# Optimization experiments

Measured on AMD Instinct MI355X. Metric: run time of the kernel, lower is better.

The kernel has to match this reference:

```python
import jax, jax.numpy as jnp
import numpy as np

N_NODES = 50000
N_EDGES = 800000
IN_C = 128
OUT_C = 128
HEADS = 1
BN_EPS = 1e-5


def setup_inputs() -> dict:
    key = jax.random.key(0)
    k1, k2, k3, k4, k5 = jax.random.split(key, 5)
    x = jax.random.normal(k1, (N_NODES, IN_C), dtype=jnp.float32)
    embedding = jax.random.normal(k2, (N_NODES, OUT_C), dtype=jnp.float32)
    # edges with no self loops (module strips then re-adds self loops)
    dst = jax.random.randint(k3, (N_EDGES,), 0, N_NODES)
    off = jax.random.randint(k4, (N_EDGES,), 1, N_NODES)
    src = (dst + off) % N_NODES
    edge_index = jnp.stack([src, dst]).astype(jnp.int64)
    # parameters
    W = jax.random.normal(k5, (HEADS * OUT_C, IN_C), dtype=jnp.float32) * (1.0 / np.sqrt(IN_C))
    bias = jnp.zeros((HEADS * OUT_C,), dtype=jnp.float32)
    gamma = jnp.ones((HEADS * OUT_C,), dtype=jnp.float32)
    beta = jnp.zeros((HEADS * OUT_C,), dtype=jnp.float32)
    return {"x": x, "edge_index": edge_index, "embedding": embedding,
            "W": W, "bias": bias, "gamma": gamma, "beta": beta}


def reference(x, edge_index, embedding, W, bias, gamma, beta):
    N = x.shape[0]
    xl = x @ W.T  # [N, H*C]
    # add self loops (input edges contain none)
    loop = jnp.arange(N, dtype=edge_index.dtype)
    src = jnp.concatenate([edge_index[0], loop])  # j (source)
    dst = jnp.concatenate([edge_index[1], loop])  # i (target / aggregation index)
    # per-edge attention: cosine-sim style embedding dot product (scalar, shared over heads)
    alpha = jnp.sum(embedding[dst] * embedding[src], axis=-1)  # [Etot]
    # segment softmax over destination neighborhoods
    amax = jax.ops.segment_max(alpha, dst, num_segments=N)
    e = jnp.exp(alpha - amax[dst])
    denom = jax.ops.segment_sum(e, dst, num_segments=N)
    a = e / (denom[dst] + 1e-16)  # [Etot]
    # gather-scale-scatter aggregation
    msg = xl[src] * a[:, None]  # [Etot, H*C]
    out = jax.ops.segment_sum(msg, dst, num_segments=N) + bias  # [N, H*C]
    # BatchNorm1d (training mode: batch stats, biased variance) + ReLU
    mu = out.mean(axis=0)
    var = jnp.mean((out - mu) ** 2, axis=0)
    out = (out - mu) * jax.lax.rsqrt(var + BN_EPS) * gamma + beta
    return jnp.maximum(out, 0.0)
```

## Files before the change

kernel.cpp:

```cpp
#include <hip/hip_runtime.h>
#include <math.h>

#define C 128

typedef _Float16 f16x8 __attribute__((ext_vector_type(8)));
typedef _Float16 half2_t __attribute__((ext_vector_type(2)));
typedef __attribute__((ext_vector_type(4))) float f32x4;

static __device__ __forceinline__ unsigned int pkh2(float lo, float hi) {
    unsigned short l = __builtin_bit_cast(unsigned short, (_Float16)lo);
    unsigned short h = __builtin_bit_cast(unsigned short, (_Float16)hi);
    return ((unsigned int)h << 16) | l;
}
static __device__ __forceinline__ float h2f_lo(unsigned int u) {
    return (float)__builtin_bit_cast(_Float16, (unsigned short)(u & 0xFFFFu));
}
static __device__ __forceinline__ float h2f_hi(unsigned int u) {
    return (float)__builtin_bit_cast(_Float16, (unsigned short)(u >> 16));
}
static __device__ __forceinline__ float dot2acc(unsigned int a, unsigned int b, float c) {
#if __has_builtin(__builtin_amdgcn_fdot2)
    return __builtin_amdgcn_fdot2(__builtin_bit_cast(half2_t, a),
                                  __builtin_bit_cast(half2_t, b), c, false);
#else
    c = fmaf(h2f_lo(a), h2f_lo(b), c);
    return fmaf(h2f_hi(a), h2f_hi(b), c);
#endif
}

__global__ __launch_bounds__(256) void k_stageA(const float* __restrict__ x,
                                                const float* __restrict__ Wf0,
                                                const uint4* __restrict__ wb,
                                                unsigned short* __restrict__ xlh,
                                                const float* __restrict__ embf,
                                                unsigned int* __restrict__ embh,
                                                unsigned int* __restrict__ Wh,
                                                const int* __restrict__ eidx,
                                                int* __restrict__ binCounts,
                                                int N, int E,
                                                int nGemmBlocks, int nCastBlocks,
                                                int totalA8, int totalB8) {
    __shared__ int lh[256];
    const int b = blockIdx.x;

    if (b < nGemmBlocks) {
        __shared__ unsigned int wsh[C * C / 2];
        const int tid = threadIdx.x;
        for (int i = tid; i < C * C / 8; i += 256) {
            const float4 a = ((const float4*)Wf0)[i * 2];
            const float4 bb = ((const float4*)Wf0)[i * 2 + 1];
            uint4 o;
            o.x = pkh2(a.x, a.y); o.y = pkh2(a.z, a.w);
            o.z = pkh2(bb.x, bb.y); o.w = pkh2(bb.z, bb.w);
            ((uint4*)wsh)[i] = o;
        }
        __syncthreads();

        const int lane = threadIdx.x & 63;
        const int wave = threadIdx.x >> 6;
        const int row0 = b * 64 + wave * 16;
        const int r = lane & 15, kg = lane >> 4;

        int arow = row0 + r;
        if (arow >= N) arow = N - 1;
        const float* xrow = x + (size_t)arow * C;
        f16x8 A[4];
#pragma unroll
        for (int kb = 0; kb < 4; ++kb) {
            const float4 p0 = ((const float4*)(xrow + kb * 32 + kg * 8))[0];
            const float4 p1 = ((const float4*)(xrow + kb * 32 + kg * 8))[1];
            f16x8 a;
            a[0] = (_Float16)p0.x; a[1] = (_Float16)p0.y;
            a[2] = (_Float16)p0.z; a[3] = (_Float16)p0.w;
            a[4] = (_Float16)p1.x; a[5] = (_Float16)p1.y;
            a[6] = (_Float16)p1.z; a[7] = (_Float16)p1.w;
            A[kb] = a;
        }

#pragma unroll
        for (int nt = 0; nt < 8; ++nt) {
            const uint4* wrow = (const uint4*)wsh + (size_t)(nt * 16 + r) * 16;
            f32x4 acc = {0.0f, 0.0f, 0.0f, 0.0f};
#pragma unroll
            for (int kb = 0; kb < 4; ++kb) {
                f16x8 B = __builtin_bit_cast(f16x8, wrow[kb * 4 + kg]);
                acc = __builtin_amdgcn_mfma_f32_16x16x32_f16(A[kb], B, acc, 0, 0, 0);
            }
            const int orow = row0 + kg * 4;
            const int ocol = nt * 16 + r;
#pragma unroll
            for (int i = 0; i < 4; ++i)
                if (orow + i < N)
                    xlh[(size_t)(orow + i) * C + ocol] =
                        __builtin_bit_cast(unsigned short, (_Float16)acc[i]);
        }
    } else if (b < nGemmBlocks + nCastBlocks) {
        int i = (b - nGemmBlocks) * 256 + threadIdx.x;
        const float* in;
        unsigned int* outp;
        if (i < totalA8) {
            in = embf; outp = embh;
        } else {
            i -= totalA8;
            if (i >= totalB8) return;
            in = Wf0; outp = Wh;
        }
        const float4 a = ((const float4*)in)[i * 2];
        const float4 bb = ((const float4*)in)[i * 2 + 1];
        uint4 o;
        o.x = pkh2(a.x, a.y); o.y = pkh2(a.z, a.w);
        o.z = pkh2(bb.x, bb.y); o.w = pkh2(bb.z, bb.w);
        ((uint4*)outp)[i] = o;
    } else {
        const int t = threadIdx.x;
        lh[t] = 0;
        __syncthreads();
        const int base = (b - nGemmBlocks - nCastBlocks) * 2048;
#pragma unroll
        for (int j = 0; j < 8; ++j) {
            const int e = base + j * 256 + t;
            if (e < E) atomicAdd(&lh[eidx[E + e] >> 8], 1);
        }
        __syncthreads();
        const int v = lh[t];
        if (v) atomicAdd(&binCounts[t], v);
    }
}

__global__ __launch_bounds__(256) void k_bin(const int* __restrict__ eidx,
                                             const int* __restrict__ binCounts,
                                             int* __restrict__ binAlloc,
                                             unsigned int* __restrict__ binned, int E) {
    __shared__ int lh[256];
    __shared__ int sc[256];
    __shared__ int lb[256];
    const int t = threadIdx.x;
    const int v = binCounts[t];
    lh[t] = 0;
    sc[t] = v;
    __syncthreads();
    const int base = blockIdx.x * 2048;
    int bj[8], rj[8];
    unsigned int recj[8];
#pragma unroll
    for (int j = 0; j < 8; ++j) {
        const int e = base + j * 256 + t;
        bj[j] = -1;
        if (e < E) {
            const int s = eidx[e];
            const int d = eidx[E + e];
            bj[j] = d >> 8;
            recj[j] = ((unsigned)(d & 255) << 24) | (unsigned)s;
            rj[j] = atomicAdd(&lh[bj[j]], 1);
        }
    }
    __syncthreads();
    for (int o = 1; o < 256; o <<= 1) {
        int u = (t >= o) ? sc[t - o] : 0;
        __syncthreads();
        sc[t] += u;
        __syncthreads();
    }
    const int excl = sc[t] - v;
    const int c = lh[t];
    if (c) lb[t] = excl + atomicAdd(&binAlloc[t], c);
    __syncthreads();
#pragma unroll
    for (int j = 0; j < 8; ++j) {
        if (bj[j] >= 0) binned[lb[bj[j]] + rj[j]] = recj[j];
    }
}

__global__ __launch_bounds__(256) void k_place(const unsigned int* __restrict__ binned,
                                               const int* __restrict__ binCounts,
                                               int* __restrict__ offs,
                                               int* __restrict__ src_s,
                                               int N, int E, int NB) {
    __shared__ int sc[256];
    __shared__ int cnt[256];
    __shared__ int ts[256];
    __shared__ int cur[256];
    __shared__ int r0s, r1s;
    const int b = blockIdx.x;
    const int t = threadIdx.x;
    const int node0 = b * 256;
    const int v0 = binCounts[t];
    sc[t] = v0;
    cnt[t] = 0;
    __syncthreads();
    for (int o = 1; o < 256; o <<= 1) {
        int u = (t >= o) ? sc[t - o] : 0;
        __syncthreads();
        sc[t] += u;
        __syncthreads();
    }
    if (t == b) { r0s = sc[t] - v0; r1s = sc[t]; }
    __syncthreads();
    const int r0 = r0s, r1 = r1s;
    for (int i = r0 + t; i < r1; i += 256)
        atomicAdd(&cnt[binned[i] >> 24], 1);
    __syncthreads();
    const int v = cnt[t];
    ts[t] = v;
    __syncthreads();
    for (int o = 1; o < 256; o <<= 1) {
        int u = (t >= o) ? ts[t - o] : 0;
        __syncthreads();
        ts[t] += u;
        __syncthreads();
    }
    const int excl = r0 + ts[t] - v;
    if (node0 + t < N) offs[node0 + t] = excl;
    cur[t] = excl;
    __syncthreads();
    for (int i = r0 + t; i < r1; i += 256) {
        const unsigned int rec = binned[i];
        const int pos = atomicAdd(&cur[rec >> 24], 1);
        src_s[pos] = (int)(rec & 0xFFFFFFu);
    }
    if (b == NB - 1 && t == 0) offs[N] = E;
}

__global__ __launch_bounds__(256) void k_agg(const unsigned int* __restrict__ xlh,
                                             const unsigned int* __restrict__ embh,
                                             const int* __restrict__ src_s,
                                             const int* __restrict__ offs,
                                             const float* __restrict__ bias,
                                             float* __restrict__ out, int N) {
    const int node = (int)((blockIdx.x * (size_t)blockDim.x + threadIdx.x) >> 6);
    const int lane = threadIdx.x & 63;
    if (node >= N) return;
    const int g = lane >> 3;
    const int sl = lane & 7;
    const int s0 = offs[node], s1 = offs[node + 1];

    const uint4* erow = (const uint4*)(embh + (size_t)node * (C / 2));
    const uint4 e0 = erow[sl * 2], e1 = erow[sl * 2 + 1];

    float p = 0.0f;
    p = dot2acc(e0.x, e0.x, p); p = dot2acc(e0.y, e0.y, p);
    p = dot2acc(e0.z, e0.z, p); p = dot2acc(e0.w, e0.w, p);
    p = dot2acc(e1.x, e1.x, p); p = dot2acc(e1.y, e1.y, p);
    p = dot2acc(e1.z, e1.z, p); p = dot2acc(e1.w, e1.w, p);
    p += __shfl_xor(p, 4); p += __shfl_xor(p, 2); p += __shfl_xor(p, 1);

    float m = p;
    float wself = 1.0f;
    float dex = 0.0f;
    float dpart = 0.0f;
    const unsigned int xw = xlh[(size_t)node * (C / 2) + lane];
    float2 acc = {h2f_lo(xw), h2f_hi(xw)};

    for (int base = s0; base < s1; base += 64) {
        int mys = -1;
        if (base + lane < s1) mys = src_s[base + lane];
        const int iters = min(8, (s1 - base + 7) >> 3);
        for (int k = 0; k < iters; ++k) {
            const int sg = __shfl(mys, k * 8 + g);
            const int sa = (sg >= 0) ? sg : node;

            const uint4* vrow = (const uint4*)(embh + (size_t)sa * (C / 2));
            const uint4 v0 = vrow[sl * 2], v1 = vrow[sl * 2 + 1];
            float a = 0.0f;
            a = dot2acc(e0.x, v0.x, a); a = dot2acc(e0.y, v0.y, a);
            a = dot2acc(e0.z, v0.z, a); a = dot2acc(e0.w, v0.w, a);
            a = dot2acc(e1.x, v1.x, a); a = dot2acc(e1.y, v1.y, a);
            a = dot2acc(e1.z, v1.z, a); a = dot2acc(e1.w, v1.w, a);
            a += __shfl_xor(a, 4); a += __shfl_xor(a, 2); a += __shfl_xor(a, 1);

            const bool valid = sg >= 0;
            const bool hot = valid && (a > m - 28.0f);
            if (__any(hot)) {
                const unsigned long long bal = __ballot(hot);
#pragma unroll 1
                for (int j = 0; j < 8; ++j) {
                    if (!((bal >> (j * 8)) & 1ULL)) continue;
                    const float aj = __shfl(a, j * 8);
                    const int sj = __shfl(mys, k * 8 + j);
                    if (aj > m) {
                        const float cs = __expf(m - aj);
                        dpart *= cs; dex *= cs; wself *= cs;
                        acc.x *= cs; acc.y *= cs;
                        m = aj;
                    }
                    const float w = __expf(aj - m);
                    dex += w;
                    if (w > 1e-12f) {
                        const unsigned int u = xlh[(size_t)sj * (C / 2) + lane];
                        acc.x = fmaf(w, h2f_lo(u), acc.x);
                        acc.y = fmaf(w, h2f_hi(u), acc.y);
                    }
                }
            }
            dpart += (valid && !hot) ? __expf(a - m) : 0.0f;
        }
    }

    float dg = dpart;
    dg += __shfl_xor(dg, 8); dg += __shfl_xor(dg, 16); dg += __shfl_xor(dg, 32);
    const float dtot = wself + dex + dg;
    const float inv = 1.0f / (dtot + 1e-16f);
    const int c = lane * 2;
    float2 o2;
    o2.x = fmaf(acc.x, inv, bias[c]);
    o2.y = fmaf(acc.y, inv, bias[c + 1]);
    ((float2*)(out + (size_t)node * C))[lane] = o2;
}

__global__ __launch_bounds__(256) void k_bnstats(const float* __restrict__ out,
                                                 float* __restrict__ ssum,
                                                 float* __restrict__ ssq, int N) {
    const int tid = threadIdx.x;
    const int total4 = N * (C / 4);
    const int stride = gridDim.x * 256;
    float4 s4 = {0, 0, 0, 0}, q4 = {0, 0, 0, 0};
    for (int i = blockIdx.x * 256 + tid; i < total4; i += stride) {
        float4 v = ((const float4*)out)[i];
        s4.x += v.x; s4.y += v.y; s4.z += v.z; s4.w += v.w;
        q4.x = fmaf(v.x, v.x, q4.x); q4.y = fmaf(v.y, v.y, q4.y);
        q4.z = fmaf(v.z, v.z, q4.z); q4.w = fmaf(v.w, v.w, q4.w);
    }
    __shared__ float4 lsum[256];
    __shared__ float4 lsq[256];
    lsum[tid] = s4; lsq[tid] = q4;
    __syncthreads();
    if (tid < 32) {
        float4 S = lsum[tid], Q = lsq[tid];
#pragma unroll
        for (int j = 1; j < 8; ++j) {
            float4 a = lsum[tid + 32 * j], b = lsq[tid + 32 * j];
            S.x += a.x; S.y += a.y; S.z += a.z; S.w += a.w;
            Q.x += b.x; Q.y += b.y; Q.z += b.z; Q.w += b.w;
        }
        const int c = tid * 4;
        atomicAdd(&ssum[c], S.x);     atomicAdd(&ssum[c + 1], S.y);
        atomicAdd(&ssum[c + 2], S.z); atomicAdd(&ssum[c + 3], S.w);
        atomicAdd(&ssq[c], Q.x);      atomicAdd(&ssq[c + 1], Q.y);
        atomicAdd(&ssq[c + 2], Q.z);  atomicAdd(&ssq[c + 3], Q.w);
    }
}

__global__ __launch_bounds__(256) void k_bnapply(float* __restrict__ out,
                                                 const float* __restrict__ ssum,
                                                 const float* __restrict__ ssq,
                                                 const float* __restrict__ gamma,
                                                 const float* __restrict__ beta,
                                                 int N) {
    const int idx = blockIdx.x * blockDim.x + threadIdx.x;
    const int total = N * (C / 4);
    if (idx >= total) return;
    const int c = (idx * 4) & 127;
    float4 v = ((const float4*)out)[idx];
    const float invN = 1.0f / (float)N;
    float r[4] = {v.x, v.y, v.z, v.w};
#pragma unroll
    for (int j = 0; j < 4; ++j) {
        float mu = ssum[c + j] * invN;
        float var = fmaf(-mu, mu, ssq[c + j] * invN);
        var = fmaxf(var, 0.0f);
        float sc = gamma[c + j] / sqrtf(var + 1e-5f);
        float val = fmaf(r[j] - mu, sc, beta[c + j]);
        r[j] = fmaxf(val, 0.0f);
    }
    float4 o = {r[0], r[1], r[2], r[3]};
    ((float4*)out)[idx] = o;
}

extern "C" void kernel_launch(void* const* d_in, const int* in_sizes, int n_in,
                              void* d_out, int out_size, void* d_ws, size_t ws_size,
                              hipStream_t stream) {
    const float* x     = (const float*)d_in[0];
    const int*   eidx  = (const int*)d_in[1];
    const float* emb   = (const float*)d_in[2];
    const float* W     = (const float*)d_in[3];
    const float* bias  = (const float*)d_in[4];
    const float* gamma = (const float*)d_in[5];
    const float* beta  = (const float*)d_in[6];
    const int N = in_sizes[0] / C;
    const int E = in_sizes[1] / 2;
    float* out = (float*)d_out;

    char* ws = (char*)d_ws;
    size_t off = 0;
    auto alloc = [&](size_t bytes) -> void* {
        void* p = ws + off;
        off = (off + bytes + 255) & ~(size_t)255;
        return p;
    };
    unsigned short* xlh  = (unsigned short*)alloc((size_t)N * C * 2);
    unsigned int*   embh = (unsigned int*)  alloc((size_t)N * C * 2);
    unsigned int*   wh   = (unsigned int*)  alloc((size_t)C * C * 2);
    int*   src_s    = (int*)  alloc((size_t)E * 4);
    unsigned int* binned = (unsigned int*)alloc((size_t)E * 4);
    int*   offs     = (int*)  alloc((size_t)(N + 1) * 4);
    char*  zbase    = (char*)alloc(0);
    int*   binCounts= (int*)  alloc(256 * 4);
    int*   binAlloc = (int*)  alloc(256 * 4);
    float* ssum     = (float*)alloc(C * 4);
    float* ssq      = (float*)alloc(C * 4);
    size_t zbytes   = (char*)ws + off - zbase;

    const int NB = (N + 255) / 256;
    const int nEdgeBlocks = (E + 2047) / 2048;
    const int embTot8 = N * (C / 8);
    const int wTot8   = C * (C / 8);
    const int nGemmBlocks = (N + 63) / 64;
    const int nCastBlocks = (embTot8 + wTot8 + 255) / 256;

    hipMemsetAsync(zbase, 0, zbytes, stream);

    k_stageA <<<nGemmBlocks + nCastBlocks + nEdgeBlocks, 256, 0, stream>>>(
                 x, W, (const uint4*)wh, xlh, emb, embh, wh, eidx, binCounts,
                 N, E, nGemmBlocks, nCastBlocks, embTot8, wTot8);
    k_bin    <<<nEdgeBlocks,     256, 0, stream>>>(eidx, binCounts, binAlloc, binned, E);
    k_place  <<<NB,              256, 0, stream>>>(binned, binCounts, offs, src_s, N, E, NB);
    k_agg    <<<(int)(((size_t)N * 64 + 255) / 256), 256, 0, stream>>>(
                 (const unsigned int*)xlh, embh, src_s, offs, bias, out, N);
    k_bnstats<<<256,             256, 0, stream>>>(out, ssum, ssq, N);
    k_bnapply<<<(N * (C / 4) + 255) / 256, 256, 0, stream>>>(out, ssum, ssq, gamma, beta, N);
}
```

Before: 136.5 us.

## Fuse BatchNorm statistics into aggregation kernel and drop unused W cast

The aggregation kernel now also builds per-block partial sums and squared sums of its outputs. These go into 64 striped slots via atomics, and a tiny reduce kernel combines them, replacing the separate stats pass that re-read the whole output. The unused fp16 cast of W in stage A is also removed. This saves one full read of the N×128 output, at the cost of a block-wide barrier and shared-memory reduction in the aggregation kernel and atomic contention on the striped slots.

```diff
diff --git a/kernel.cpp b/kernel.cpp
--- a/kernel.cpp
+++ b/kernel.cpp
@@ -30,16 +30,14 @@
 
 __global__ __launch_bounds__(256) void k_stageA(const float* __restrict__ x,
                                                 const float* __restrict__ Wf0,
-                                                const uint4* __restrict__ wb,
                                                 unsigned short* __restrict__ xlh,
                                                 const float* __restrict__ embf,
                                                 unsigned int* __restrict__ embh,
-                                                unsigned int* __restrict__ Wh,
                                                 const int* __restrict__ eidx,
                                                 int* __restrict__ binCounts,
                                                 int N, int E,
                                                 int nGemmBlocks, int nCastBlocks,
-                                                int totalA8, int totalB8) {
+                                                int totalA8) {
     __shared__ int lh[256];
     const int b = blockIdx.x;
 
@@ -96,21 +94,13 @@
         }
     } else if (b < nGemmBlocks + nCastBlocks) {
         int i = (b - nGemmBlocks) * 256 + threadIdx.x;
-        const float* in;
-        unsigned int* outp;
-        if (i < totalA8) {
-            in = embf; outp = embh;
-        } else {
-            i -= totalA8;
-            if (i >= totalB8) return;
-            in = Wf0; outp = Wh;
-        }
-        const float4 a = ((const float4*)in)[i * 2];
-        const float4 bb = ((const float4*)in)[i * 2 + 1];
+        if (i >= totalA8) return;
+        const float4 a = ((const float4*)embf)[i * 2];
+        const float4 bb = ((const float4*)embf)[i * 2 + 1];
         uint4 o;
         o.x = pkh2(a.x, a.y); o.y = pkh2(a.z, a.w);
         o.z = pkh2(bb.x, bb.y); o.w = pkh2(bb.z, bb.w);
-        ((uint4*)outp)[i] = o;
+        ((uint4*)embh)[i] = o;
     } else {
         const int t = threadIdx.x;
         lh[t] = 0;
@@ -226,118 +216,130 @@
                                              const int* __restrict__ src_s,
                                              const int* __restrict__ offs,
                                              const float* __restrict__ bias,
-                                             float* __restrict__ out, int N) {
+                                             float* __restrict__ out,
+                                             float* __restrict__ psum,
+                                             float* __restrict__ psq, int N) {
     const int node = (int)((blockIdx.x * (size_t)blockDim.x + threadIdx.x) >> 6);
     const int lane = threadIdx.x & 63;
-    if (node >= N) return;
-    const int g = lane >> 3;
-    const int sl = lane & 7;
-    const int s0 = offs[node], s1 = offs[node + 1];
-
-    const uint4* erow = (const uint4*)(embh + (size_t)node * (C / 2));
-    const uint4 e0 = erow[sl * 2], e1 = erow[sl * 2 + 1];
-
-    float p = 0.0f;
-    p = dot2acc(e0.x, e0.x, p); p = dot2acc(e0.y, e0.y, p);
-    p = dot2acc(e0.z, e0.z, p); p = dot2acc(e0.w, e0.w, p);
-    p = dot2acc(e1.x, e1.x, p); p = dot2acc(e1.y, e1.y, p);
-    p = dot2acc(e1.z, e1.z, p); p = dot2acc(e1.w, e1.w, p);
-    p += __shfl_xor(p, 4); p += __shfl_xor(p, 2); p += __shfl_xor(p, 1);
-
-    float m = p;
-    float wself = 1.0f;
-    float dex = 0.0f;
-    float dpart = 0.0f;
-    const unsigned int xw = xlh[(size_t)node * (C / 2) + lane];
-    float2 acc = {h2f_lo(xw), h2f_hi(xw)};
-
-    for (int base = s0; base < s1; base += 64) {
-        int mys = -1;
-        if (base + lane < s1) mys = src_s[base + lane];
-        const int iters = min(8, (s1 - base + 7) >> 3);
-        for (int k = 0; k < iters; ++k) {
-            const int sg = __shfl(mys, k * 8 + g);
-            const int sa = (sg >= 0) ? sg : node;
-
-            const uint4* vrow = (const uint4*)(embh + (size_t)sa * (C / 2));
-            const uint4 v0 = vrow[sl * 2], v1 = vrow[sl * 2 + 1];
-            float a = 0.0f;
-            a = dot2acc(e0.x, v0.x, a); a = dot2acc(e0.y, v0.y, a);
-            a = dot2acc(e0.z, v0.z, a); a = dot2acc(e0.w, v0.w, a);
-            a = dot2acc(e1.x, v1.x, a); a = dot2acc(e1.y, v1.y, a);
-            a = dot2acc(e1.z, v1.z, a); a = dot2acc(e1.w, v1.w, a);
-            a += __shfl_xor(a, 4); a += __shfl_xor(a, 2); a += __shfl_xor(a, 1);
-
-            const bool valid = sg >= 0;
-            const bool hot = valid && (a > m - 28.0f);
-            if (__any(hot)) {
-                const unsigned long long bal = __ballot(hot);
+    const int wave = threadIdx.x >> 6;
+    const bool active = node < N;
+    float2 o2 = {0.0f, 0.0f};
+
+    if (active) {
+        const int g = lane >> 3;
+        const int sl = lane & 7;
+        const int s0 = offs[node], s1 = offs[node + 1];
+
+        const uint4* erow = (const uint4*)(embh + (size_t)node * (C / 2));
+        const uint4 e0 = erow[sl * 2], e1 = erow[sl * 2 + 1];
+
+        float p = 0.0f;
+        p = dot2acc(e0.x, e0.x, p); p = dot2acc(e0.y, e0.y, p);
+        p = dot2acc(e0.z, e0.z, p); p = dot2acc(e0.w, e0.w, p);
+        p = dot2acc(e1.x, e1.x, p); p = dot2acc(e1.y, e1.y, p);
+        p = dot2acc(e1.z, e1.z, p); p = dot2acc(e1.w, e1.w, p);
+        p += __shfl_xor(p, 4); p += __shfl_xor(p, 2); p += __shfl_xor(p, 1);
+
+        float m = p;
+        float wself = 1.0f;
+        float dex = 0.0f;
+        float dpart = 0.0f;
+        const unsigned int xw = xlh[(size_t)node * (C / 2) + lane];
+        float2 acc = {h2f_lo(xw), h2f_hi(xw)};
+
+        for (int base = s0; base < s1; base += 64) {
+            int mys = -1;
+            if (base + lane < s1) mys = src_s[base + lane];
+            const int iters = min(8, (s1 - base + 7) >> 3);
+            for (int k = 0; k < iters; ++k) {
+                const int sg = __shfl(mys, k * 8 + g);
+                const int sa = (sg >= 0) ? sg : node;
+
+                const uint4* vrow = (const uint4*)(embh + (size_t)sa * (C / 2));
+                const uint4 v0 = vrow[sl * 2], v1 = vrow[sl * 2 + 1];
+                float a = 0.0f;
+                a = dot2acc(e0.x, v0.x, a); a = dot2acc(e0.y, v0.y, a);
+                a = dot2acc(e0.z, v0.z, a); a = dot2acc(e0.w, v0.w, a);
+                a = dot2acc(e1.x, v1.x, a); a = dot2acc(e1.y, v1.y, a);
+                a = dot2acc(e1.z, v1.z, a); a = dot2acc(e1.w, v1.w, a);
+                a += __shfl_xor(a, 4); a += __shfl_xor(a, 2); a += __shfl_xor(a, 1);
+
+                const bool valid = sg >= 0;
+                const bool hot = valid && (a > m - 28.0f);
+                if (__any(hot)) {
+                    const unsigned long long bal = __ballot(hot);
 #pragma unroll 1
-                for (int j = 0; j < 8; ++j) {
-                    if (!((bal >> (j * 8)) & 1ULL)) continue;
-                    const float aj = __shfl(a, j * 8);
-                    const int sj = __shfl(mys, k * 8 + j);
-                    if (aj > m) {
-                        const float cs = __expf(m - aj);
-                        dpart *= cs; dex *= cs; wself *= cs;
-                        acc.x *= cs; acc.y *= cs;
-                        m = aj;
-                    }
-                    const float w = __expf(aj - m);
-                    dex += w;
-                    if (w > 1e-12f) {
-                        const unsigned int u = xlh[(size_t)sj * (C / 2) + lane];
-                        acc.x = fmaf(w, h2f_lo(u), acc.x);
-                        acc.y = fmaf(w, h2f_hi(u), acc.y);
+                    for (int j = 0; j < 8; ++j) {
+                        if (!((bal >> (j * 8)) & 1ULL)) continue;
+                        const float aj = __shfl(a, j * 8);
+                        const int sj = __shfl(mys, k * 8 + j);
+                        if (aj > m) {
+                            const float cs = __expf(m - aj);
+                            dpart *= cs; dex *= cs; wself *= cs;
+                            acc.x *= cs; acc.y *= cs;
+                            m = aj;
+                        }
+                        const float w = __expf(aj - m);
+                        dex += w;
+                        if (w > 1e-12f) {
+                            const unsigned int u = xlh[(size_t)sj * (C / 2) + lane];
+                            acc.x = fmaf(w, h2f_lo(u), acc.x);
+                            acc.y = fmaf(w, h2f_hi(u), acc.y);
+                        }
                     }
                 }
+                dpart += (valid && !hot) ? __expf(a - m) : 0.0f;
             }
-            dpart += (valid && !hot) ? __expf(a - m) : 0.0f;
-        }
-    }
-
-    float dg = dpart;
-    dg += __shfl_xor(dg, 8); dg += __shfl_xor(dg, 16); dg += __shfl_xor(dg, 32);
-    const float dtot = wself + dex + dg;
-    const float inv = 1.0f / (dtot + 1e-16f);
-    const int c = lane * 2;
-    float2 o2;
-    o2.x = fmaf(acc.x, inv, bias[c]);
-    o2.y = fmaf(acc.y, inv, bias[c + 1]);
-    ((float2*)(out + (size_t)node * C))[lane] = o2;
-}
-
-__global__ __launch_bounds__(256) void k_bnstats(const float* __restrict__ out,
-                                                 float* __restrict__ ssum,
-                                                 float* __restrict__ ssq, int N) {
-    const int tid = threadIdx.x;
-    const int total4 = N * (C / 4);
-    const int stride = gridDim.x * 256;
-    float4 s4 = {0, 0, 0, 0}, q4 = {0, 0, 0, 0};
-    for (int i = blockIdx.x * 256 + tid; i < total4; i += stride) {
-        float4 v = ((const float4*)out)[i];
-        s4.x += v.x; s4.y += v.y; s4.z += v.z; s4.w += v.w;
-        q4.x = fmaf(v.x, v.x, q4.x); q4.y = fmaf(v.y, v.y, q4.y);
-        q4.z = fmaf(v.z, v.z, q4.z); q4.w = fmaf(v.w, v.w, q4.w);
-    }
-    __shared__ float4 lsum[256];
-    __shared__ float4 lsq[256];
-    lsum[tid] = s4; lsq[tid] = q4;
-    __syncthreads();
-    if (tid < 32) {
-        float4 S = lsum[tid], Q = lsq[tid];
-#pragma unroll
-        for (int j = 1; j < 8; ++j) {
-            float4 a = lsum[tid + 32 * j], b = lsq[tid + 32 * j];
-            S.x += a.x; S.y += a.y; S.z += a.z; S.w += a.w;
-            Q.x += b.x; Q.y += b.y; Q.z += b.z; Q.w += b.w;
-        }
-        const int c = tid * 4;
-        atomicAdd(&ssum[c], S.x);     atomicAdd(&ssum[c + 1], S.y);
-        atomicAdd(&ssum[c + 2], S.z); atomicAdd(&ssum[c + 3], S.w);
-        atomicAdd(&ssq[c], Q.x);      atomicAdd(&ssq[c + 1], Q.y);
-        atomicAdd(&ssq[c + 2], Q.z);  atomicAdd(&ssq[c + 3], Q.w);
-    }
+        }
+
+        float dg = dpart;
+        dg += __shfl_xor(dg, 8); dg += __shfl_xor(dg, 16); dg += __shfl_xor(dg, 32);
+        const float dtot = wself + dex + dg;
+        const float inv = 1.0f / (dtot + 1e-16f);
+        const int c = lane * 2;
+        o2.x = fmaf(acc.x, inv, bias[c]);
+        o2.y = fmaf(acc.y, inv, bias[c + 1]);
+        ((float2*)(out + (size_t)node * C))[lane] = o2;
+    }
+
+    __shared__ float2 lsum[256];
+    __shared__ float2 lsq[256];
+    lsum[threadIdx.x] = o2;
+    float2 q2v;
+    q2v.x = o2.x * o2.x;
+    q2v.y = o2.y * o2.y;
+    lsq[threadIdx.x] = q2v;
+    __syncthreads();
+    if (wave == 0) {
+        float2 S = lsum[lane], Q = lsq[lane];
+#pragma unroll
+        for (int j = 1; j < 4; ++j) {
+            const float2 a = lsum[j * 64 + lane];
+            const float2 b = lsq[j * 64 + lane];
+            S.x += a.x; S.y += a.y;
+            Q.x += b.x; Q.y += b.y;
+        }
+        const int slot = ((int)blockIdx.x & 63) * C + lane * 2;
+        atomicAdd(&psum[slot],     S.x);
+        atomicAdd(&psum[slot + 1], S.y);
+        atomicAdd(&psq[slot],      Q.x);
+        atomicAdd(&psq[slot + 1],  Q.y);
+    }
+}
+
+__global__ __launch_bounds__(128) void k_bnreduce(const float* __restrict__ psum,
+                                                  const float* __restrict__ psq,
+                                                  float* __restrict__ ssum,
+                                                  float* __restrict__ ssq) {
+    const int t = threadIdx.x;
+    float S = 0.0f, Q = 0.0f;
+#pragma unroll 4
+    for (int b = 0; b < 64; ++b) {
+        S += psum[b * C + t];
+        Q += psq[b * C + t];
+    }
+    ssum[t] = S;
+    ssq[t] = Q;
 }
 
 __global__ __launch_bounds__(256) void k_bnapply(float* __restrict__ out,
@@ -389,33 +391,34 @@
     };
     unsigned short* xlh  = (unsigned short*)alloc((size_t)N * C * 2);
     unsigned int*   embh = (unsigned int*)  alloc((size_t)N * C * 2);
-    unsigned int*   wh   = (unsigned int*)  alloc((size_t)C * C * 2);
     int*   src_s    = (int*)  alloc((size_t)E * 4);
     unsigned int* binned = (unsigned int*)alloc((size_t)E * 4);
     int*   offs     = (int*)  alloc((size_t)(N + 1) * 4);
+    float* ssum     = (float*)alloc(C * 4);
+    float* ssq      = (float*)alloc(C * 4);
     char*  zbase    = (char*)alloc(0);
     int*   binCounts= (int*)  alloc(256 * 4);
     int*   binAlloc = (int*)  alloc(256 * 4);
-    float* ssum     = (float*)alloc(C * 4);
-    float* ssq      = (float*)alloc(C * 4);
+    float* psum     = (float*)alloc(64 * C * 4);
+    float* psq      = (float*)alloc(64 * C * 4);
     size_t zbytes   = (char*)ws + off - zbase;
 
     const int NB = (N + 255) / 256;
     const int nEdgeBlocks = (E + 2047) / 2048;
     const int embTot8 = N * (C / 8);
-    const int wTot8   = C * (C / 8);
     const int nGemmBlocks = (N + 63) / 64;
-    const int nCastBlocks = (embTot8 + wTot8 + 255) / 256;
+    const int nCastBlocks = (embTot8 + 255) / 256;
 
     hipMemsetAsync(zbase, 0, zbytes, stream);
 
     k_stageA <<<nGemmBlocks + nCastBlocks + nEdgeBlocks, 256, 0, stream>>>(
-                 x, W, (const uint4*)wh, xlh, emb, embh, wh, eidx, binCounts,
-                 N, E, nGemmBlocks, nCastBlocks, embTot8, wTot8);
+                 x, W, xlh, emb, embh, eidx, binCounts,
+                 N, E, nGemmBlocks, nCastBlocks, embTot8);
     k_bin    <<<nEdgeBlocks,     256, 0, stream>>>(eidx, binCounts, binAlloc, binned, E);
     k_place  <<<NB,              256, 0, stream>>>(binned, binCounts, offs, src_s, N, E, NB);
     k_agg    <<<(int)(((size_t)N * 64 + 255) / 256), 256, 0, stream>>>(
-                 (const unsigned int*)xlh, embh, src_s, offs, bias, out, N);
-    k_bnstats<<<256,             256, 0, stream>>>(out, ssum, ssq, N);
+                 (const unsigned int*)xlh, embh, src_s, offs, bias, out,
+                 psum, psq, N);
+    k_bnreduce<<<1,              128, 0, stream>>>(psum, psq, ssum, ssq);
     k_bnapply<<<(N * (C / 4) + 255) / 256, 256, 0, stream>>>(out, ssum, ssq, gamma, beta, N);
 }
```

New measurement: 121.2 us. 1.13x faster.
